# Optimization experiments

Measured on AMD Instinct MI355X. Metric: run time of the kernel, lower is better.

## Reference

```python
import jax, jax.numpy as jnp
import numpy as np

NUM_HEADS = 16


def setup_inputs() -> dict:
    key = jax.random.key(0)
    k1, k2, k3 = jax.random.split(key, 3)
    B, S, C = 1, 4096, 1024
    x = jax.random.normal(k1, (B, S, C), dtype=jnp.float32)
    # additive causal mask: 0 on/below diagonal, -1e9 above
    causal = jnp.triu(jnp.full((S, S), -1e9, dtype=jnp.float32), k=1)
    attention_mask = causal[None, None, :, :]
    W_attn = jax.random.normal(k2, (C, 3 * C), dtype=jnp.float32) * (C ** -0.5)
    b_attn = jnp.zeros((3 * C,), dtype=jnp.float32)
    W_proj = jax.random.normal(k3, (C, C), dtype=jnp.float32) * (C ** -0.5)
    b_proj = jnp.zeros((C,), dtype=jnp.float32)
    return {"x": x, "attention_mask": attention_mask, "W_attn": W_attn,
            "b_attn": b_attn, "W_proj": W_proj, "b_proj": b_proj}


def reference(x, attention_mask, W_attn, b_attn, W_proj, b_proj):
    B, S, C = x.shape
    H = NUM_HEADS
    hd = C // H
    qkv = x @ W_attn + b_attn                      # [B,S,3C]
    q, k, v = jnp.split(qkv, 3, axis=-1)
    # [B,S,C] -> [B,H,S,hd]
    q = q.reshape(B, S, H, hd).transpose(0, 2, 1, 3)
    k = k.reshape(B, S, H, hd).transpose(0, 2, 1, 3)
    v = v.reshape(B, S, H, hd).transpose(0, 2, 1, 3)
    att = jnp.einsum('bhqd,bhkd->bhqk', q, k) / jnp.sqrt(jnp.float32(hd))
    att = att + attention_mask                     # additive causal mask
    att = jax.nn.softmax(att, axis=-1)             # dropout is identity (p=0/eval)
    out = jnp.einsum('bhqk,bhkd->bhqd', att, v)    # [B,H,S,hd]
    out = out.transpose(0, 2, 1, 3).reshape(B, S, C)
    return out @ W_proj + b_proj
```

## Files before the change

kernel.cpp:

```cpp
#include <hip/hip_runtime.h>
#include <stdint.h>


typedef __bf16 bf16x8 __attribute__((ext_vector_type(8)));
typedef float f32x4 __attribute__((ext_vector_type(4)));

#define QSCALE 0.18033688011112042f

__device__ __forceinline__ f32x4 mfma16(bf16x8 a, bf16x8 b, f32x4 c) {
  return __builtin_amdgcn_mfma_f32_16x16x32_bf16(a, b, c, 0, 0, 0);
}

__device__ __forceinline__ void g2l16(const void* g, void* l) {
  __builtin_amdgcn_global_load_lds(
      (const __attribute__((address_space(1))) unsigned int*)g,
      (__attribute__((address_space(3))) unsigned int*)l,
      16, 0, 0);
}

__device__ __forceinline__ uint16_t f2bf(float f) {
  unsigned int u = __builtin_bit_cast(unsigned int, f);
  u += 0x7fffu + ((u >> 16) & 1u);
  return (uint16_t)(u >> 16);
}

__device__ __forceinline__ unsigned int pack_hi(float lo, float hi) {
  return __builtin_amdgcn_perm(__builtin_bit_cast(unsigned int, hi),
                               __builtin_bit_cast(unsigned int, lo), 0x07060302u);
}

__global__ __launch_bounds__(256) void f2b_k(const float* __restrict__ in,
                                             uint16_t* __restrict__ out, int n) {
  const int base = (blockIdx.x * 256 + threadIdx.x) * 8;
  if (base >= n) return;
  float4 a = *(const float4*)(in + base);
  float4 b = *(const float4*)(in + base + 4);
  uint16_t t[8];
  t[0] = f2bf(a.x); t[1] = f2bf(a.y); t[2] = f2bf(a.z); t[3] = f2bf(a.w);
  t[4] = f2bf(b.x); t[5] = f2bf(b.y); t[6] = f2bf(b.z); t[7] = f2bf(b.w);
  *(int4*)(out + base) = *(const int4*)t;
}

__global__ __launch_bounds__(256) void transpose2_f2b(const float* __restrict__ inA,
                                                      uint16_t* __restrict__ outA,
                                                      const float* __restrict__ inB,
                                                      uint16_t* __restrict__ outB) {
  __shared__ float t[64][65];
  const int tx = threadIdx.x & 15;
  const int ty = threadIdx.x >> 4;
  const bool isA = blockIdx.x < 48;
  const float* in = isA ? inA : inB;
  uint16_t* out = isA ? outA : outB;
  const int C = isA ? 3072 : 1024;
  const int bx = isA ? blockIdx.x : (blockIdx.x - 48);
  const int r0 = blockIdx.y * 64, c0 = bx * 64;
#pragma unroll
  for (int rr = ty; rr < 64; rr += 16) {
    float4 v = *(const float4*)(in + (size_t)(r0 + rr) * C + c0 + tx * 4);
    t[rr][tx * 4 + 0] = v.x; t[rr][tx * 4 + 1] = v.y;
    t[rr][tx * 4 + 2] = v.z; t[rr][tx * 4 + 3] = v.w;
  }
  __syncthreads();
#pragma unroll
  for (int cc = ty; cc < 64; cc += 16) {
    uint16_t tmp[4];
#pragma unroll
    for (int j = 0; j < 4; j++) tmp[j] = f2bf(t[tx * 4 + j][cc]);
    *(uint2*)(out + (size_t)(c0 + cc) * 1024 + r0 + tx * 4) = *(const uint2*)tmp;
  }
}

template <int EPI>
__global__ __launch_bounds__(256) void gemm_bt(const uint16_t* __restrict__ A,
                                               const uint16_t* __restrict__ Bt,
                                               const float* __restrict__ bias,
                                               uint16_t* __restrict__ outQ,
                                               uint16_t* __restrict__ outK,
                                               uint16_t* __restrict__ outV,
                                               float* __restrict__ outF) {
  __shared__ __align__(16) uint16_t lA[128 * 32];
  __shared__ __align__(16) uint16_t lB[128 * 32];
  const int tid = threadIdx.x;
  const int w = tid >> 6, lane = tid & 63;
  const int quad = lane >> 4, c16 = lane & 15;
  const int m0 = blockIdx.y * 128, n0 = blockIdx.x * 128;

  f32x4 acc[4][4];
#pragma unroll
  for (int i = 0; i < 4; i++)
#pragma unroll
    for (int j = 0; j < 4; j++) acc[i][j] = f32x4{0.f, 0.f, 0.f, 0.f};

  for (int k0 = 0; k0 < 1024; k0 += 32) {
    __syncthreads();
#pragma unroll
    for (int ii = 0; ii < 2; ii++) {
      const int instr = w * 2 + ii;
      const int p16 = instr * 64 + lane;
      const int row = p16 >> 2, cp = p16 & 3;
      const int c = cp ^ ((row >> 1) & 3);
      g2l16(A + (size_t)(m0 + row) * 1024 + k0 + c * 8, (char*)lA + (size_t)instr * 1024);
      g2l16(Bt + (size_t)(n0 + row) * 1024 + k0 + c * 8, (char*)lB + (size_t)instr * 1024);
    }
    __syncthreads();
    bf16x8 af[4], bfr[4];
#pragma unroll
    for (int t = 0; t < 4; t++) {
      const int mr = (w >> 1) * 64 + t * 16 + c16;
      af[t] = *(const bf16x8*)((const char*)lA + mr * 64 + ((quad ^ ((mr >> 1) & 3)) * 16));
      const int nr = (w & 1) * 64 + t * 16 + c16;
      bfr[t] = *(const bf16x8*)((const char*)lB + nr * 64 + ((quad ^ ((nr >> 1) & 3)) * 16));
    }
#pragma unroll
    for (int i = 0; i < 4; i++)
#pragma unroll
      for (int j = 0; j < 4; j++) acc[i][j] = mfma16(af[i], bfr[j], acc[i][j]);
  }

  const int mbase = m0 + (w >> 1) * 64;
  const int nbase = n0 + (w & 1) * 64;
  float bv[4];
#pragma unroll
  for (int j = 0; j < 4; j++) bv[j] = bias[nbase + j * 16 + c16];
#pragma unroll
  for (int i = 0; i < 4; i++) {
#pragma unroll
    for (int j = 0; j < 4; j++) {
      const int n = nbase + j * 16 + c16;
#pragma unroll
      for (int r = 0; r < 4; r++) {
        const int m = mbase + i * 16 + quad * 4 + r;
        float fv = acc[i][j][r] + bv[j];
        if (EPI == 0) {
          const int region = n >> 10;
          const int cr = n & 1023;
          const int h = cr >> 6, d = cr & 63;
          if (region == 0)      outQ[((size_t)(h << 12) + m) * 64 + d] = f2bf(fv * QSCALE);
          else if (region == 1) outK[((size_t)(h << 12) + m) * 64 + d] = f2bf(fv);
          else                  outV[(((size_t)(h * 32 + (m >> 7)) * 64 + d) << 7) + (m & 127)] = f2bf(fv);
        } else {
          outF[(size_t)m * 1024 + n] = fv;
        }
      }
    }
  }
}

__global__ __launch_bounds__(64, 2) void attn_kernel(const uint16_t* __restrict__ Qb,
                                                     const uint16_t* __restrict__ Kb,
                                                     const uint16_t* __restrict__ Vtb,
                                                     float* __restrict__ Op,
                                                     float* __restrict__ lb) {
  __shared__ __align__(16) uint16_t lP[64 * 128];
  const int lane = threadIdx.x;
  const int quad = lane >> 4, c16 = lane & 15;
  const int bid = blockIdx.x;
  const int w = bid >> 10;
  const int r = bid & 1023;
  const int h = r & 15;
  const int sw = 63 - (r >> 4);
  const int q0w = sw * 64;
  const int jmax = sw >> 1;

  bf16x8 qf[4][2];
#pragma unroll
  for (int ntq = 0; ntq < 4; ntq++)
#pragma unroll
    for (int kc = 0; kc < 2; kc++) {
      int4 v = *(const int4*)(Qb + ((size_t)(h << 12) + q0w + ntq * 16 + c16) * 64 + kc * 32 + quad * 8);
      qf[ntq][kc] = __builtin_bit_cast(bf16x8, v);
    }

  float ls[4] = {0.f, 0.f, 0.f, 0.f};
  f32x4 o[4][4];
#pragma unroll
  for (int i = 0; i < 4; i++)
#pragma unroll
    for (int nq = 0; nq < 4; nq++) o[i][nq] = f32x4{0.f, 0.f, 0.f, 0.f};

  for (int j = w; j <= jmax; j += 2) {
    const uint16_t* kbase = Kb + ((size_t)(h << 12) + j * 128) * 64;

#pragma unroll
    for (int half = 0; half < 2; half++) {
      int4 kf[2][4];
#pragma unroll
      for (int kc = 0; kc < 2; kc++)
#pragma unroll
        for (int mt = 0; mt < 4; mt++)
          kf[kc][mt] = *(const int4*)(kbase + (half * 64 + mt * 16 + c16) * 64 + kc * 32 + quad * 8);

#pragma unroll
      for (int qp = 0; qp < 2; qp++) {
        f32x4 st[4][2];
#pragma unroll
        for (int mt = 0; mt < 4; mt++) { st[mt][0] = f32x4{0.f,0.f,0.f,0.f}; st[mt][1] = f32x4{0.f,0.f,0.f,0.f}; }
#pragma unroll
        for (int kc = 0; kc < 2; kc++)
#pragma unroll
          for (int mt = 0; mt < 4; mt++) {
            bf16x8 a = __builtin_bit_cast(bf16x8, kf[kc][mt]);
            st[mt][0] = mfma16(a, qf[qp * 2 + 0][kc], st[mt][0]);
            st[mt][1] = mfma16(a, qf[qp * 2 + 1][kc], st[mt][1]);
          }

        if (j == jmax) {
#pragma unroll
          for (int nt = 0; nt < 2; nt++) {
            const int qg = q0w + qp * 32 + nt * 16 + c16;
#pragma unroll
            for (int mt = 0; mt < 4; mt++)
#pragma unroll
              for (int rr = 0; rr < 4; rr++) {
                const int key = j * 128 + half * 64 + mt * 16 + quad * 4 + rr;
                if (key > qg) st[mt][nt][rr] = -1.0e9f;
              }
          }
        }

#pragma unroll
        for (int nt = 0; nt < 2; nt++) {
          float sum0 = 0.f, sum1 = 0.f;
          const int prow = qp * 32 + nt * 16 + c16;
          const size_t pbase = (size_t)prow * 256;
#pragma unroll
          for (int mt = 0; mt < 4; mt++) {
            float p0 = __builtin_amdgcn_exp2f(st[mt][nt][0]);
            float p1 = __builtin_amdgcn_exp2f(st[mt][nt][1]);
            float p2 = __builtin_amdgcn_exp2f(st[mt][nt][2]);
            float p3 = __builtin_amdgcn_exp2f(st[mt][nt][3]);
            sum0 += p0 + p1;
            sum1 += p2 + p3;
            const unsigned int lo = pack_hi(p0, p1);
            const unsigned int hi = pack_hi(p2, p3);
            const int chunk = half * 8 + mt * 2 + (quad >> 1);
            uint2* dst = (uint2*)((char*)lP + pbase + ((chunk ^ (prow & 15)) << 4) + (quad & 1) * 8);
            *dst = make_uint2(lo, hi);
          }
          float sum = sum0 + sum1;
          sum += __shfl_xor(sum, 16);
          sum += __shfl_xor(sum, 32);
          ls[qp * 2 + nt] += sum;
        }
      }
    }

    const uint16_t* vbase = Vtb + (((size_t)(h * 32 + j) * 64) << 7);
#pragma unroll
    for (int kc = 0; kc < 4; kc++) {
      int4 vf[4];
#pragma unroll
      for (int mt = 0; mt < 4; mt++)
        vf[mt] = *(const int4*)(vbase + ((mt * 16 + c16) << 7) + (kc * 4 + quad) * 8);
      bf16x8 pb[4];
#pragma unroll
      for (int ntq = 0; ntq < 4; ntq++) {
        const int prow = ntq * 16 + c16;
        const int chunk = kc * 4 + quad;
        pb[ntq] = *(const bf16x8*)((const char*)lP + (size_t)prow * 256 +
                                   ((chunk ^ (prow & 15)) << 4));
      }
#pragma unroll
      for (int mt = 0; mt < 4; mt++) {
        bf16x8 a = __builtin_bit_cast(bf16x8, vf[mt]);
#pragma unroll
        for (int ntq = 0; ntq < 4; ntq++)
          o[mt][ntq] = mfma16(a, pb[ntq], o[mt][ntq]);
      }
    }
  }

  float* Opw = Op + (((size_t)(w * 16 + h)) << 12) * 64;
  float* lbw = lb + (((size_t)(w * 16 + h)) << 12);
#pragma unroll
  for (int ntq = 0; ntq < 4; ntq++) {
    const int qg = q0w + ntq * 16 + c16;
#pragma unroll
    for (int mt = 0; mt < 4; mt++)
      *(f32x4*)(Opw + (size_t)qg * 64 + mt * 16 + quad * 4) = o[mt][ntq];
    if (quad == 0) lbw[qg] = ls[ntq];
  }
}

__global__ __launch_bounds__(256) void combine_k(const float* __restrict__ Op,
                                                 const float* __restrict__ lb,
                                                 uint16_t* __restrict__ Ob) {
  const int e = blockIdx.x * 256 + threadIdx.x;
  const int q = e >> 8;
  const int rem = e & 255;
  const int h = rem >> 4;
  const int dg = (rem & 15) << 2;
  const float* p0 = Op + (((size_t)h << 12) + q) * 64 + dg;
  const float* p1 = Op + (((size_t)(16 + h) << 12) + q) * 64 + dg;
  const float l = lb[((size_t)h << 12) + q] + lb[((size_t)(16 + h) << 12) + q];
  const float4 a = *(const float4*)p0;
  const float4 b = *(const float4*)p1;
  const float inv = 1.f / l;
  uint16_t t[4];
  t[0] = f2bf((a.x + b.x) * inv);
  t[1] = f2bf((a.y + b.y) * inv);
  t[2] = f2bf((a.z + b.z) * inv);
  t[3] = f2bf((a.w + b.w) * inv);
  *(uint2*)(Ob + (size_t)q * 1024 + h * 64 + dg) = *(const uint2*)t;
}

extern "C" void kernel_launch(void* const* d_in, const int* in_sizes, int n_in,
                              void* d_out, int out_size, void* d_ws, size_t ws_size,
                              hipStream_t stream) {
  const float* x      = (const float*)d_in[0];
  const float* W_attn = (const float*)d_in[2];
  const float* b_attn = (const float*)d_in[3];
  const float* W_proj = (const float*)d_in[4];
  const float* b_proj = (const float*)d_in[5];
  float* out = (float*)d_out;

  char* ws = (char*)d_ws;
  uint16_t* Ob  = (uint16_t*)(ws);
  uint16_t* wtA = (uint16_t*)(ws + 8388608);
  uint16_t* wtP = (uint16_t*)(ws + 14680064);
  uint16_t* Qb  = (uint16_t*)(ws + 16777216);
  uint16_t* Kb  = (uint16_t*)(ws + 25165824);
  uint16_t* Vtb = (uint16_t*)(ws + 33554432);
  uint16_t* xb  = (uint16_t*)(ws + 41943040);
  float*    Op  = (float*)(ws + 50331648);
  float*    lb  = (float*)(ws + 83886080);

  f2b_k<<<2048, 256, 0, stream>>>(x, xb, 4096 * 1024);
  transpose2_f2b<<<dim3(64, 16), 256, 0, stream>>>(W_attn, wtA, W_proj, wtP);
  gemm_bt<0><<<dim3(24, 32), 256, 0, stream>>>(xb, wtA, b_attn, Qb, Kb, Vtb, nullptr);
  attn_kernel<<<dim3(2048), 64, 0, stream>>>(Qb, Kb, Vtb, Op, lb);
  combine_k<<<dim3(4096), 256, 0, stream>>>(Op, lb, Ob);
  gemm_bt<1><<<dim3(8, 32), 256, 0, stream>>>(Ob, wtP, b_proj, nullptr, nullptr, nullptr, out);
}
```

Baseline: 278.4 us.

## Split attention KV range across four waves per block and combine in LDS

The attention kernel now launches one 256-thread block per (head, query tile) with four waves, each handling every fourth KV block, instead of two separate single-wave blocks. Partial outputs and row sums are reduced through shared memory inside the block, and the normalized bf16 output is written directly. This removes the separate combine kernel, its launch, and the fp32 partial-output round trip through global memory. In exchange each block uses four times the LDS, a block barrier is added, and the causal split over four waves can leave waves unevenly loaded on short query tiles.

```diff
diff --git a/kernel.cpp b/kernel.cpp
--- a/kernel.cpp
+++ b/kernel.cpp
@@ -146,19 +146,19 @@
   }
 }
 
-__global__ __launch_bounds__(64, 2) void attn_kernel(const uint16_t* __restrict__ Qb,
-                                                     const uint16_t* __restrict__ Kb,
-                                                     const uint16_t* __restrict__ Vtb,
-                                                     float* __restrict__ Op,
-                                                     float* __restrict__ lb) {
-  __shared__ __align__(16) uint16_t lP[64 * 128];
-  const int lane = threadIdx.x;
+__global__ __launch_bounds__(256, 2) void attn_kernel(const uint16_t* __restrict__ Qb,
+                                                      const uint16_t* __restrict__ Kb,
+                                                      const uint16_t* __restrict__ Vtb,
+                                                      uint16_t* __restrict__ Ob) {
+  __shared__ __align__(16) uint16_t lP[4][64 * 128];
+  __shared__ float lL[4][64];
+  const int tid = threadIdx.x;
+  const int w = tid >> 6;
+  const int lane = tid & 63;
   const int quad = lane >> 4, c16 = lane & 15;
   const int bid = blockIdx.x;
-  const int w = bid >> 10;
-  const int r = bid & 1023;
-  const int h = r & 15;
-  const int sw = 63 - (r >> 4);
+  const int h = bid & 15;
+  const int sw = 63 - (bid >> 4);
   const int q0w = sw * 64;
   const int jmax = sw >> 1;
 
@@ -178,7 +178,7 @@
 #pragma unroll
     for (int nq = 0; nq < 4; nq++) o[i][nq] = f32x4{0.f, 0.f, 0.f, 0.f};
 
-  for (int j = w; j <= jmax; j += 2) {
+  for (int j = w; j <= jmax; j += 4) {
     const uint16_t* kbase = Kb + ((size_t)(h << 12) + j * 128) * 64;
 
 #pragma unroll
@@ -234,7 +234,7 @@
             const unsigned int lo = pack_hi(p0, p1);
             const unsigned int hi = pack_hi(p2, p3);
             const int chunk = half * 8 + mt * 2 + (quad >> 1);
-            uint2* dst = (uint2*)((char*)lP + pbase + ((chunk ^ (prow & 15)) << 4) + (quad & 1) * 8);
+            uint2* dst = (uint2*)((char*)lP[w] + pbase + ((chunk ^ (prow & 15)) << 4) + (quad & 1) * 8);
             *dst = make_uint2(lo, hi);
           }
           float sum = sum0 + sum1;
@@ -257,7 +257,7 @@
       for (int ntq = 0; ntq < 4; ntq++) {
         const int prow = ntq * 16 + c16;
         const int chunk = kc * 4 + quad;
-        pb[ntq] = *(const bf16x8*)((const char*)lP + (size_t)prow * 256 +
+        pb[ntq] = *(const bf16x8*)((const char*)lP[w] + (size_t)prow * 256 +
                                    ((chunk ^ (prow & 15)) << 4));
       }
 #pragma unroll
@@ -270,38 +270,35 @@
     }
   }
 
-  float* Opw = Op + (((size_t)(w * 16 + h)) << 12) * 64;
-  float* lbw = lb + (((size_t)(w * 16 + h)) << 12);
-#pragma unroll
-  for (int ntq = 0; ntq < 4; ntq++) {
-    const int qg = q0w + ntq * 16 + c16;
-#pragma unroll
-    for (int mt = 0; mt < 4; mt++)
-      *(f32x4*)(Opw + (size_t)qg * 64 + mt * 16 + quad * 4) = o[mt][ntq];
-    if (quad == 0) lbw[qg] = ls[ntq];
-  }
-}
-
-__global__ __launch_bounds__(256) void combine_k(const float* __restrict__ Op,
-                                                 const float* __restrict__ lb,
-                                                 uint16_t* __restrict__ Ob) {
-  const int e = blockIdx.x * 256 + threadIdx.x;
-  const int q = e >> 8;
-  const int rem = e & 255;
-  const int h = rem >> 4;
-  const int dg = (rem & 15) << 2;
-  const float* p0 = Op + (((size_t)h << 12) + q) * 64 + dg;
-  const float* p1 = Op + (((size_t)(16 + h) << 12) + q) * 64 + dg;
-  const float l = lb[((size_t)h << 12) + q] + lb[((size_t)(16 + h) << 12) + q];
-  const float4 a = *(const float4*)p0;
-  const float4 b = *(const float4*)p1;
-  const float inv = 1.f / l;
-  uint16_t t[4];
-  t[0] = f2bf((a.x + b.x) * inv);
-  t[1] = f2bf((a.y + b.y) * inv);
-  t[2] = f2bf((a.z + b.z) * inv);
-  t[3] = f2bf((a.w + b.w) * inv);
-  *(uint2*)(Ob + (size_t)q * 1024 + h * 64 + dg) = *(const uint2*)t;
+  float* oL = (float*)lP[w];
+#pragma unroll
+  for (int mt = 0; mt < 4; mt++)
+#pragma unroll
+    for (int ntq = 0; ntq < 4; ntq++)
+#pragma unroll
+      for (int rr = 0; rr < 4; rr++)
+        oL[(mt * 16 + quad * 4 + rr) * 64 + ntq * 16 + c16] = o[mt][ntq][rr];
+  if (quad == 0) {
+#pragma unroll
+    for (int ntq = 0; ntq < 4; ntq++) lL[w][ntq * 16 + c16] = ls[ntq];
+  }
+  __syncthreads();
+
+  const int q = tid & 63, dq = tid >> 6;
+  const float lsum = lL[0][q] + lL[1][q] + lL[2][q] + lL[3][q];
+  const float inv = 1.f / lsum;
+  uint16_t t[16] __attribute__((aligned(16)));
+#pragma unroll
+  for (int i = 0; i < 16; i++) {
+    const int d = dq * 16 + i;
+    const int off = d * 64 + q;
+    float s = ((const float*)lP[0])[off] + ((const float*)lP[1])[off] +
+              ((const float*)lP[2])[off] + ((const float*)lP[3])[off];
+    t[i] = f2bf(s * inv);
+  }
+  uint16_t* dst = Ob + (size_t)(q0w + q) * 1024 + h * 64 + dq * 16;
+  *(int4*)dst = *(const int4*)t;
+  *(int4*)(dst + 8) = *(const int4*)(t + 8);
 }
 
 extern "C" void kernel_launch(void* const* d_in, const int* in_sizes, int n_in,
@@ -322,13 +319,10 @@
   uint16_t* Kb  = (uint16_t*)(ws + 25165824);
   uint16_t* Vtb = (uint16_t*)(ws + 33554432);
   uint16_t* xb  = (uint16_t*)(ws + 41943040);
-  float*    Op  = (float*)(ws + 50331648);
-  float*    lb  = (float*)(ws + 83886080);
 
   f2b_k<<<2048, 256, 0, stream>>>(x, xb, 4096 * 1024);
   transpose2_f2b<<<dim3(64, 16), 256, 0, stream>>>(W_attn, wtA, W_proj, wtP);
   gemm_bt<0><<<dim3(24, 32), 256, 0, stream>>>(xb, wtA, b_attn, Qb, Kb, Vtb, nullptr);
-  attn_kernel<<<dim3(2048), 64, 0, stream>>>(Qb, Kb, Vtb, Op, lb);
-  combine_k<<<dim3(4096), 256, 0, stream>>>(Op, lb, Ob);
+  attn_kernel<<<dim3(1024), 256, 0, stream>>>(Qb, Kb, Vtb, Ob);
   gemm_bt<1><<<dim3(8, 32), 256, 0, stream>>>(Ob, wtP, b_proj, nullptr, nullptr, nullptr, out);
 }
```

New measurement: 262.0 us. 1.06x faster.
